# Performance work log

Hardware: AMD Instinct MI355X
Metric: run time of the kernel (lower is better)

## Reference

```python
import jax, jax.numpy as jnp
import numpy as np

N = 100000   # nodes
E = 1200000  # directed edges (avg degree 12)
D = 64       # in_feats
C = 40       # n_classes
K = 16       # propagation steps
ALPHA = 0.05


def setup_inputs() -> dict:
    key = jax.random.key(0)
    k1, k2, k3, k4 = jax.random.split(key, 4)
    feat = jax.random.normal(k1, (N, D), jnp.float32)
    # xavier_uniform for fc.weight [C, D]
    limit = np.sqrt(6.0 / (D + C)).astype(np.float32)
    W = jax.random.uniform(k2, (C, D), jnp.float32, -limit, limit)
    b = jnp.zeros((C,), jnp.float32)
    src = jax.random.randint(k3, (E,), 0, N, dtype=jnp.int32)
    dst = jax.random.randint(k4, (E,), 0, N, dtype=jnp.int32)
    return {"feat": feat, "W": W, "b": b, "src": src, "dst": dst}


def reference(feat, W, b, src, dst):
    # --- getNormAugAdj: A_hat = D^{-1/2} (A + I) D^{-1/2} ---
    loops = jnp.arange(N, dtype=src.dtype)
    row = jnp.concatenate([dst, loops])  # output node of each edge
    col = jnp.concatenate([src, loops])  # input  node of each edge
    ones = jnp.ones(row.shape, feat.dtype)
    deg = jax.ops.segment_sum(ones, row, num_segments=N)  # >= 1 (self-loops)
    dinv = jax.lax.rsqrt(deg)
    w = dinv[row] * dinv[col]  # per-edge normalized weight

    def spmm(x):  # x: [N, D] -> A_hat @ x
        return jax.ops.segment_sum(w[:, None] * x[col], row, num_segments=N)

    feat_ori = feat

    # SSGC loop (faithful to the original, including h /= K inside the loop)
    def step(carry, _):
        x, h = carry
        x = spmm(x)
        h = (h + (1.0 - ALPHA) * x + ALPHA * feat_ori) / K
        return (x, h), None

    (_, h), _ = jax.lax.scan(step, (feat, jnp.zeros_like(feat)), None, length=K)

    # fc(h)
    return h @ W.T + b
```

## Files before the change

### kernel.cpp

```cpp
#include <hip/hip_runtime.h>
#include <hip/hip_fp16.h>

#define NN 100000
#define EE 1200000
#define DD 64
#define CC 40
#define KK 16
#define BSZ 196
#define NBK 512
#define TCAP 3072
#define EPB 4096
#define ABLK ((EE + EPB - 1) / EPB)
#define PL1 (NN * 4)
#define GBLK ((NN + 11) / 12)

struct __align__(8) ERec { int c; float w; };

__global__ __launch_bounds__(512) void curinit_kernel(int* __restrict__ cursor) {
    int b = threadIdx.x;
    if (b < NBK) cursor[b] = b * TCAP;
}

__global__ __launch_bounds__(256) void sortA_kernel(const int* __restrict__ src,
                                                    const int* __restrict__ dst,
                                                    int* __restrict__ cursor,
                                                    int2* __restrict__ tmp) {
    __shared__ int2 stg[EPB];
    __shared__ int hist[NBK], loff[NBK], lcur[NBK], gbase[NBK];
    int t = threadIdx.x;
    long e0 = (long)blockIdx.x * EPB;
    int n = (int)((EE - e0 < EPB) ? (EE - e0) : EPB);
    for (int j = t; j < NBK; j += 256) hist[j] = 0;
    __syncthreads();
    int d[16], sx[16];
#pragma unroll
    for (int j = 0; j < 16; ++j) {
        int i = t + j * 256;
        if (i < n) {
            d[j] = dst[e0 + i];
            sx[j] = src[e0 + i];
            atomicAdd(&hist[d[j] / BSZ], 1);
        } else d[j] = -1;
    }
    __syncthreads();
    int c0 = hist[2 * t], c1 = hist[2 * t + 1];
    int s2 = c0 + c1;
    __syncthreads();
    loff[t] = s2;
    __syncthreads();
    for (int off = 1; off < 256; off <<= 1) {
        int u = (t >= off) ? loff[t - off] : 0;
        __syncthreads();
        loff[t] += u;
        __syncthreads();
    }
    int excl = loff[t] - s2;
    __syncthreads();
    loff[2 * t] = excl;          loff[2 * t + 1] = excl + c0;
    lcur[2 * t] = excl;          lcur[2 * t + 1] = excl + c0;
    gbase[2 * t]     = atomicAdd(&cursor[2 * t], c0);
    gbase[2 * t + 1] = atomicAdd(&cursor[2 * t + 1], c1);
    __syncthreads();
#pragma unroll
    for (int j = 0; j < 16; ++j) {
        if (d[j] >= 0) {
            int b = d[j] / BSZ;
            int p = atomicAdd(&lcur[b], 1);
            stg[p] = make_int2(d[j], sx[j]);
        }
    }
    __syncthreads();
    for (int i = t; i < n; i += 256) {
        int2 r = stg[i];
        int b = r.x / BSZ;
        int pos = gbase[b] + (i - loff[b]);
        if (pos < (b + 1) * TCAP) tmp[pos] = r;
    }
}

__global__ __launch_bounds__(512) void bscan_kernel(const int* __restrict__ cursor,
                                                    int* __restrict__ bbase,
                                                    int* __restrict__ row_ptr) {
    __shared__ int sm[512];
    int t = threadIdx.x;
    int v = (t < NBK) ? (cursor[t] - t * TCAP) : 0;
    sm[t] = v;
    __syncthreads();
    for (int off = 1; off < 512; off <<= 1) {
        int u = (t >= off) ? sm[t - off] : 0;
        __syncthreads();
        sm[t] += u;
        __syncthreads();
    }
    if (t < NBK) bbase[t] = sm[t] - v;
    if (t == 511) row_ptr[NN] = sm[511];
}

__global__ __launch_bounds__(256) void sortB_kernel(const int2* __restrict__ tmp,
                                                    const int* __restrict__ cursor,
                                                    const int* __restrict__ bbase,
                                                    float* __restrict__ dinv,
                                                    int* __restrict__ row_ptr,
                                                    int2* __restrict__ er2) {
    __shared__ int2 se[TCAP];
    __shared__ int2 so[TCAP];
    __shared__ int hist[256], lcur[256];
    int b = blockIdx.x;
    int n0 = b * BSZ;
    if (n0 >= NN) return;
    int n1 = n0 + BSZ; if (n1 > NN) n1 = NN;
    int nb = n1 - n0;
    int t = threadIdx.x;
    int cnt = cursor[b] - b * TCAP;
    int base = bbase[b];
    hist[t] = 0;
    __syncthreads();
    for (int i = t; i < cnt; i += 256) {
        int2 r = tmp[b * TCAP + i];
        se[i] = r;
        atomicAdd(&hist[r.x - n0], 1);
    }
    __syncthreads();
    if (t < nb) dinv[n0 + t] = rsqrtf((float)(hist[t] + 1));
    int v = hist[t];
    lcur[t] = v;
    __syncthreads();
    for (int off = 1; off < 256; off <<= 1) {
        int u = (t >= off) ? lcur[t - off] : 0;
        __syncthreads();
        lcur[t] += u;
        __syncthreads();
    }
    int excl = lcur[t] - v;
    __syncthreads();
    lcur[t] = excl;
    if (t < nb) row_ptr[n0 + t] = base + excl;
    __syncthreads();
    for (int i = t; i < cnt; i += 256) {
        int2 r = se[i];
        int ln = r.x - n0;
        int pos = atomicAdd(&lcur[ln], 1);
        so[pos] = make_int2(r.y, r.x);
    }
    __syncthreads();
    for (int i = t; i < cnt; i += 256) er2[base + i] = so[i];
}

__global__ __launch_bounds__(256) void wfill_kernel(const int2* __restrict__ er2,
                                                    const float* __restrict__ dinv,
                                                    int2* __restrict__ er) {
    int i = blockIdx.x * 256 + threadIdx.x;
    if (i >= EE) return;
    int2 r = er2[i];
    float w = dinv[r.y] * dinv[r.x];
    er[i] = make_int2(r.x, __float_as_int(w));
}

__global__ __launch_bounds__(256) void proj_kernel(const float4* __restrict__ feat4,
                                                   const float* __restrict__ W,
                                                   float4* __restrict__ y0) {
    __shared__ float smW[CC * 68];
    __shared__ float smF[64 * 68];
    __shared__ float smO[64 * 42];
    int t = threadIdx.x;
    for (int j = t; j < CC * 16; j += 256) {
        int c = j >> 4, q = j & 15;
        *(float4*)(smW + c * 68 + q * 4) = ((const float4*)W)[j];
    }
    int n0 = blockIdx.x * 64;
    for (int j = t; j < 64 * 16; j += 256) {
        int r = j >> 4, q = j & 15;
        if (n0 + r < NN)
            *(float4*)(smF + r * 68 + q * 4) = feat4[(size_t)(n0 + r) * 16 + q];
    }
    __syncthreads();
    int ln = t >> 2, c0 = (t & 3) * 10;
    int node = n0 + ln;
    float acc[10];
#pragma unroll
    for (int c = 0; c < 10; ++c) acc[c] = 0.f;
    if (node < NN) {
#pragma unroll
        for (int db = 0; db < 16; ++db) {
            float4 fv = *(const float4*)(smF + ln * 68 + db * 4);
#pragma unroll
            for (int c = 0; c < 10; ++c) {
                float4 wv = *(const float4*)(smW + (c0 + c) * 68 + db * 4);
                acc[c] = fmaf(fv.x, wv.x, acc[c]);
                acc[c] = fmaf(fv.y, wv.y, acc[c]);
                acc[c] = fmaf(fv.z, wv.z, acc[c]);
                acc[c] = fmaf(fv.w, wv.w, acc[c]);
            }
        }
    }
#pragma unroll
    for (int c = 0; c < 10; ++c) smO[ln * 42 + c0 + c] = acc[c];
    __syncthreads();
    for (int j = t; j < 64 * 5; j += 256) {
        int r = j / 5, q = j - r * 5;
        if (n0 + r < NN) {
            const float* s = smO + r * 42 + q * 8;
            float4 ov;
            __half2* op = (__half2*)&ov;
            op[0] = __floats2half2_rn(s[0], s[1]);
            op[1] = __floats2half2_rn(s[2], s[3]);
            op[2] = __floats2half2_rn(s[4], s[5]);
            op[3] = __floats2half2_rn(s[6], s[7]);
            y0[(q < 4) ? ((size_t)(n0 + r) * 4 + q) : (size_t)(PL1 + n0 + r)] = ov;
        }
    }
}

#define DEC8(V, F0, F1, F2, F3)                                             \
    const __half2* hp_##F0 = (const __half2*)&(V);                          \
    float2 F0 = __half22float2(hp_##F0[0]), F1 = __half22float2(hp_##F0[1]);\
    float2 F2 = __half22float2(hp_##F0[2]), F3 = __half22float2(hp_##F0[3]);

#define ACC8(R, V)                                                          \
    {                                                                       \
        DEC8(V, f0, f1, f2, f3)                                             \
        a0 = fmaf((R).w, f0.x, a0); a1 = fmaf((R).w, f0.y, a1);             \
        a2 = fmaf((R).w, f1.x, a2); a3 = fmaf((R).w, f1.y, a3);             \
        a4 = fmaf((R).w, f2.x, a4); a5 = fmaf((R).w, f2.y, a5);             \
        a6 = fmaf((R).w, f3.x, a6); a7 = fmaf((R).w, f3.y, a7);             \
    }

#define EDGE_LOOP                                                           \
    int e = beg;                                                            \
    int e8 = beg + ((end - beg) & ~7);                                      \
    for (; e < e8; e += 8) {                                                \
        ERec r0 = er[e], r1 = er[e + 1], r2 = er[e + 2], r3 = er[e + 3];    \
        ERec r4 = er[e + 4], r5 = er[e + 5], r6 = er[e + 6], r7 = er[e + 7];\
        float4 v0 = x[r0.c * m + a];                                        \
        float4 v1 = x[r1.c * m + a];                                        \
        float4 v2 = x[r2.c * m + a];                                        \
        float4 v3 = x[r3.c * m + a];                                        \
        float4 v4 = x[r4.c * m + a];                                        \
        float4 v5 = x[r5.c * m + a];                                        \
        float4 v6 = x[r6.c * m + a];                                        \
        float4 v7 = x[r7.c * m + a];                                        \
        ACC8(r0, v0); ACC8(r1, v1); ACC8(r2, v2); ACC8(r3, v3);             \
        ACC8(r4, v4); ACC8(r5, v5); ACC8(r6, v6); ACC8(r7, v7);             \
    }                                                                       \
    int e4 = e + ((end - e) & ~3);                                          \
    for (; e < e4; e += 4) {                                                \
        ERec r0 = er[e], r1 = er[e + 1], r2 = er[e + 2], r3 = er[e + 3];    \
        float4 v0 = x[r0.c * m + a];                                        \
        float4 v1 = x[r1.c * m + a];                                        \
        float4 v2 = x[r2.c * m + a];                                        \
        float4 v3 = x[r3.c * m + a];                                        \
        ACC8(r0, v0); ACC8(r1, v1); ACC8(r2, v2); ACC8(r3, v3);             \
    }                                                                       \
    for (; e < end; ++e) {                                                  \
        ERec r = er[e];                                                     \
        float4 v = x[r.c * m + a];                                          \
        ACC8(r, v);                                                         \
    }

__global__ __launch_bounds__(64) void spmm_prop(
    const float4* __restrict__ x, float4* __restrict__ x_out,
    const int* __restrict__ row_ptr, const ERec* __restrict__ er,
    const float* __restrict__ dinv) {
    int lane = threadIdx.x;
    int nw = lane / 5;
    int li = lane - nw * 5;
    int g = blockIdx.x * 12 + nw;
    if (nw >= 12 || g >= NN) return;
    int beg = row_ptr[g], end = row_ptr[g + 1];
    float di = dinv[g];
    float w0 = di * di;
    int m = (li < 4) ? 4 : 1;
    int a = (li < 4) ? li : PL1;
    int base = g * m + a;
    float4 sv = x[base];
    float a0, a1, a2, a3, a4, a5, a6, a7;
    {
        DEC8(sv, f0, f1, f2, f3)
        a0 = w0 * f0.x; a1 = w0 * f0.y; a2 = w0 * f1.x; a3 = w0 * f1.y;
        a4 = w0 * f2.x; a5 = w0 * f2.y; a6 = w0 * f3.x; a7 = w0 * f3.y;
    }
    EDGE_LOOP
    float4 ov;
    __half2* op = (__half2*)&ov;
    op[0] = __floats2half2_rn(a0, a1);
    op[1] = __floats2half2_rn(a2, a3);
    op[2] = __floats2half2_rn(a4, a5);
    op[3] = __floats2half2_rn(a6, a7);
    x_out[base] = ov;
}

__global__ __launch_bounds__(64) void spmm_final(
    const float4* __restrict__ x,
    const float4* __restrict__ x13p,
    const float4* __restrict__ x14p,
    const float4* __restrict__ y0,
    const float* __restrict__ bias,
    const int* __restrict__ row_ptr, const ERec* __restrict__ er,
    const float* __restrict__ dinv, float* __restrict__ outp) {
    int lane = threadIdx.x;
    int nw = lane / 5;
    int li = lane - nw * 5;
    int g = blockIdx.x * 12 + nw;
    if (nw >= 12 || g >= NN) return;
    int beg = row_ptr[g], end = row_ptr[g + 1];
    float di = dinv[g];
    float w0 = di * di;
    int m = (li < 4) ? 4 : 1;
    int a = (li < 4) ? li : PL1;
    int base = g * m + a;
    float4 sv = x[base];
    float s0, s1, s2, s3, s4, s5, s6, s7;
    float a0, a1, a2, a3, a4, a5, a6, a7;
    {
        DEC8(sv, f0, f1, f2, f3)
        s0 = f0.x; s1 = f0.y; s2 = f1.x; s3 = f1.y;
        s4 = f2.x; s5 = f2.y; s6 = f3.x; s7 = f3.y;
        a0 = w0 * s0; a1 = w0 * s1; a2 = w0 * s2; a3 = w0 * s3;
        a4 = w0 * s4; a5 = w0 * s5; a6 = w0 * s6; a7 = w0 * s7;
    }
    EDGE_LOOP
    const float C16 = 0.95f / 16.0f;
    const float C15 = 0.95f / 256.0f;
    const float C14 = 0.95f / 4096.0f;
    const float C13 = 0.95f / 65536.0f;
    const float FC  = 0.05f / 15.0f;
    float o0 = C16 * a0 + C15 * s0, o1 = C16 * a1 + C15 * s1;
    float o2 = C16 * a2 + C15 * s2, o3 = C16 * a3 + C15 * s3;
    float o4 = C16 * a4 + C15 * s4, o5 = C16 * a5 + C15 * s5;
    float o6 = C16 * a6 + C15 * s6, o7 = C16 * a7 + C15 * s7;
#define ADD8(P, CF)                                                         \
    {                                                                       \
        float4 v = (P)[base];                                               \
        DEC8(v, f0, f1, f2, f3)                                             \
        o0 = fmaf((CF), f0.x, o0); o1 = fmaf((CF), f0.y, o1);               \
        o2 = fmaf((CF), f1.x, o2); o3 = fmaf((CF), f1.y, o3);               \
        o4 = fmaf((CF), f2.x, o4); o5 = fmaf((CF), f2.y, o5);               \
        o6 = fmaf((CF), f3.x, o6); o7 = fmaf((CF), f3.y, o7);               \
    }
    ADD8(x14p, C14)
    ADD8(x13p, C13)
    ADD8(y0, FC)
#undef ADD8
    const float4* b4 = (const float4*)(bias + li * 8);
    float4 bb0 = b4[0], bb1 = b4[1];
    float4 w0v = make_float4(o0 + bb0.x, o1 + bb0.y, o2 + bb0.z, o3 + bb0.w);
    float4 w1v = make_float4(o4 + bb1.x, o5 + bb1.y, o6 + bb1.z, o7 + bb1.w);
    float4* op = (float4*)(outp + (size_t)g * CC + li * 8);
    op[0] = w0v; op[1] = w1v;
}

extern "C" void kernel_launch(void* const* d_in, const int* in_sizes, int n_in,
                              void* d_out, int out_size, void* d_ws, size_t ws_size,
                              hipStream_t stream) {
    const float* feat = (const float*)d_in[0];
    const float* W    = (const float*)d_in[1];
    const float* b    = (const float*)d_in[2];
    const int*   src  = (const int*)d_in[3];
    const int*   dst  = (const int*)d_in[4];
    float* out = (float*)d_out;

    char* p = (char*)d_ws;
    auto alloc = [&](size_t bytes) {
        char* r = p;
        p += (bytes + 255) & ~(size_t)255;
        return r;
    };
    float*   dinv    = (float*)alloc((size_t)NN * sizeof(float));
    int*     row_ptr = (int*)alloc((size_t)(NN + 1) * sizeof(int));
    int*     cursor  = (int*)alloc((size_t)NBK * sizeof(int));
    int*     bbase   = (int*)alloc((size_t)NBK * sizeof(int));
    int2*    tmp     = (int2*)alloc((size_t)NBK * TCAP * sizeof(int2));
    int2*    er2     = (int2*)alloc((size_t)EE * sizeof(int2));
    int2*    er      = (int2*)alloc((size_t)EE * sizeof(int2));
    float4*  y0      = (float4*)alloc((size_t)NN * 5 * sizeof(float4));
    float4*  xa      = (float4*)alloc((size_t)NN * 5 * sizeof(float4));
    float4*  xb      = (float4*)alloc((size_t)NN * 5 * sizeof(float4));
    float4*  x13b    = (float4*)alloc((size_t)NN * 5 * sizeof(float4));
    float4*  x14b    = (float4*)alloc((size_t)NN * 5 * sizeof(float4));
    float4*  x15b    = (float4*)alloc((size_t)NN * 5 * sizeof(float4));

    curinit_kernel<<<1, 512, 0, stream>>>(cursor);
    sortA_kernel<<<ABLK, 256, 0, stream>>>(src, dst, cursor, tmp);
    bscan_kernel<<<1, 512, 0, stream>>>(cursor, bbase, row_ptr);
    sortB_kernel<<<NBK, 256, 0, stream>>>(tmp, cursor, bbase, dinv, row_ptr, er2);
    wfill_kernel<<<(EE + 255) / 256, 256, 0, stream>>>(er2, dinv, er);
    proj_kernel<<<(NN + 63) / 64, 256, 0, stream>>>((const float4*)feat, W, y0);

    const float4* xs = y0;
    for (int j = 0; j < 12; ++j) {
        float4* xd = (j & 1) ? xb : xa;
        spmm_prop<<<GBLK, 64, 0, stream>>>(xs, xd, row_ptr, (const ERec*)er, dinv);
        xs = xd;
    }
    spmm_prop<<<GBLK, 64, 0, stream>>>(xs, x13b, row_ptr, (const ERec*)er, dinv);
    spmm_prop<<<GBLK, 64, 0, stream>>>(x13b, x14b, row_ptr, (const ERec*)er, dinv);
    spmm_prop<<<GBLK, 64, 0, stream>>>(x14b, x15b, row_ptr, (const ERec*)er, dinv);
    spmm_final<<<GBLK, 64, 0, stream>>>(x15b, x13b, x14b, y0, b, row_ptr,
                                        (const ERec*)er, dinv, out);
}
```

Measured before the change: 583.4 us.

## Split projected features into five column-plane arrays and remap SpMM blocks per plane

Stores the 40-wide half-precision projected features as five separate planes of 16-byte chunks, one per group of 8 classes, instead of four interleaved chunks plus a fifth plane. SpMM blocks now handle a plane pair (32 nodes × 2 chunks) or the last plane alone (64 nodes), instead of packing 12 nodes × 5 lanes into a 64-wide wave that left 4 lanes idle. The aim is full wave utilization and a smaller gather footprint per plane, which should help cache locality. The cost is that each edge's index and weight records are read separately per plane, so edge-list traffic goes up and rows of very different degree can share a wave.

```diff
diff --git a/kernel.cpp b/kernel.cpp
--- a/kernel.cpp
+++ b/kernel.cpp
@@ -11,8 +11,10 @@
 #define TCAP 3072
 #define EPB 4096
 #define ABLK ((EE + EPB - 1) / EPB)
-#define PL1 (NN * 4)
-#define GBLK ((NN + 11) / 12)
+
+#define NB2 3125
+#define NB1 1563
+#define GBLK2 (2 * NB2 + NB1)
 
 struct __align__(8) ERec { int c; float w; };
 
@@ -197,7 +199,7 @@
     for (int c = 0; c < 10; ++c) smO[ln * 42 + c0 + c] = acc[c];
     __syncthreads();
     for (int j = t; j < 64 * 5; j += 256) {
-        int r = j / 5, q = j - r * 5;
+        int r = j & 63, q = j >> 6;
         if (n0 + r < NN) {
             const float* s = smO + r * 42 + q * 8;
             float4 ov;
@@ -206,7 +208,7 @@
             op[1] = __floats2half2_rn(s[2], s[3]);
             op[2] = __floats2half2_rn(s[4], s[5]);
             op[3] = __floats2half2_rn(s[6], s[7]);
-            y0[(q < 4) ? ((size_t)(n0 + r) * 4 + q) : (size_t)(PL1 + n0 + r)] = ov;
+            y0[(size_t)q * NN + (n0 + r)] = ov;
         }
     }
 }
@@ -225,68 +227,75 @@
         a6 = fmaf((R).w, f3.x, a6); a7 = fmaf((R).w, f3.y, a7);             \
     }
 
-#define EDGE_LOOP                                                           \
+#define EDGE_LOOP(XP)                                                       \
     int e = beg;                                                            \
     int e8 = beg + ((end - beg) & ~7);                                      \
     for (; e < e8; e += 8) {                                                \
         ERec r0 = er[e], r1 = er[e + 1], r2 = er[e + 2], r3 = er[e + 3];    \
         ERec r4 = er[e + 4], r5 = er[e + 5], r6 = er[e + 6], r7 = er[e + 7];\
-        float4 v0 = x[r0.c * m + a];                                        \
-        float4 v1 = x[r1.c * m + a];                                        \
-        float4 v2 = x[r2.c * m + a];                                        \
-        float4 v3 = x[r3.c * m + a];                                        \
-        float4 v4 = x[r4.c * m + a];                                        \
-        float4 v5 = x[r5.c * m + a];                                        \
-        float4 v6 = x[r6.c * m + a];                                        \
-        float4 v7 = x[r7.c * m + a];                                        \
+        float4 v0 = (XP)[r0.c];                                             \
+        float4 v1 = (XP)[r1.c];                                             \
+        float4 v2 = (XP)[r2.c];                                             \
+        float4 v3 = (XP)[r3.c];                                             \
+        float4 v4 = (XP)[r4.c];                                             \
+        float4 v5 = (XP)[r5.c];                                             \
+        float4 v6 = (XP)[r6.c];                                             \
+        float4 v7 = (XP)[r7.c];                                             \
         ACC8(r0, v0); ACC8(r1, v1); ACC8(r2, v2); ACC8(r3, v3);             \
         ACC8(r4, v4); ACC8(r5, v5); ACC8(r6, v6); ACC8(r7, v7);             \
     }                                                                       \
     int e4 = e + ((end - e) & ~3);                                          \
     for (; e < e4; e += 4) {                                                \
         ERec r0 = er[e], r1 = er[e + 1], r2 = er[e + 2], r3 = er[e + 3];    \
-        float4 v0 = x[r0.c * m + a];                                        \
-        float4 v1 = x[r1.c * m + a];                                        \
-        float4 v2 = x[r2.c * m + a];                                        \
-        float4 v3 = x[r3.c * m + a];                                        \
+        float4 v0 = (XP)[r0.c];                                             \
+        float4 v1 = (XP)[r1.c];                                             \
+        float4 v2 = (XP)[r2.c];                                             \
+        float4 v3 = (XP)[r3.c];                                             \
         ACC8(r0, v0); ACC8(r1, v1); ACC8(r2, v2); ACC8(r3, v3);             \
     }                                                                       \
     for (; e < end; ++e) {                                                  \
         ERec r = er[e];                                                     \
-        float4 v = x[r.c * m + a];                                          \
+        float4 v = (XP)[r.c];                                               \
         ACC8(r, v);                                                         \
     }
+
+__device__ __forceinline__ bool bmap(int b, int lane, int& g, int& q) {
+    if (b < 2 * NB2) {
+        int pb = (b >= NB2) ? 1 : 0;
+        g = (b - pb * NB2) * 32 + (lane >> 1);
+        q = pb * 2 + (lane & 1);
+        return true;
+    }
+    g = (b - 2 * NB2) * 64 + lane;
+    q = 4;
+    return g < NN;
+}
 
 __global__ __launch_bounds__(64) void spmm_prop(
     const float4* __restrict__ x, float4* __restrict__ x_out,
     const int* __restrict__ row_ptr, const ERec* __restrict__ er,
     const float* __restrict__ dinv) {
-    int lane = threadIdx.x;
-    int nw = lane / 5;
-    int li = lane - nw * 5;
-    int g = blockIdx.x * 12 + nw;
-    if (nw >= 12 || g >= NN) return;
+    int g, q;
+    if (!bmap(blockIdx.x, threadIdx.x, g, q)) return;
+    const float4* xp = x + (size_t)q * NN;
     int beg = row_ptr[g], end = row_ptr[g + 1];
     float di = dinv[g];
     float w0 = di * di;
-    int m = (li < 4) ? 4 : 1;
-    int a = (li < 4) ? li : PL1;
-    int base = g * m + a;
-    float4 sv = x[base];
+    float4 sv = xp[g];
     float a0, a1, a2, a3, a4, a5, a6, a7;
     {
         DEC8(sv, f0, f1, f2, f3)
         a0 = w0 * f0.x; a1 = w0 * f0.y; a2 = w0 * f1.x; a3 = w0 * f1.y;
         a4 = w0 * f2.x; a5 = w0 * f2.y; a6 = w0 * f3.x; a7 = w0 * f3.y;
     }
-    EDGE_LOOP
+    EDGE_LOOP(xp)
     float4 ov;
     __half2* op = (__half2*)&ov;
     op[0] = __floats2half2_rn(a0, a1);
     op[1] = __floats2half2_rn(a2, a3);
     op[2] = __floats2half2_rn(a4, a5);
     op[3] = __floats2half2_rn(a6, a7);
-    x_out[base] = ov;
+    x_out[(size_t)q * NN + g] = ov;
 }
 
 __global__ __launch_bounds__(64) void spmm_final(
@@ -297,18 +306,14 @@
     const float* __restrict__ bias,
     const int* __restrict__ row_ptr, const ERec* __restrict__ er,
     const float* __restrict__ dinv, float* __restrict__ outp) {
-    int lane = threadIdx.x;
-    int nw = lane / 5;
-    int li = lane - nw * 5;
-    int g = blockIdx.x * 12 + nw;
-    if (nw >= 12 || g >= NN) return;
+    int g, q;
+    if (!bmap(blockIdx.x, threadIdx.x, g, q)) return;
+    const float4* xp = x + (size_t)q * NN;
+    size_t idx = (size_t)q * NN + g;
     int beg = row_ptr[g], end = row_ptr[g + 1];
     float di = dinv[g];
     float w0 = di * di;
-    int m = (li < 4) ? 4 : 1;
-    int a = (li < 4) ? li : PL1;
-    int base = g * m + a;
-    float4 sv = x[base];
+    float4 sv = xp[g];
     float s0, s1, s2, s3, s4, s5, s6, s7;
     float a0, a1, a2, a3, a4, a5, a6, a7;
     {
@@ -318,7 +323,7 @@
         a0 = w0 * s0; a1 = w0 * s1; a2 = w0 * s2; a3 = w0 * s3;
         a4 = w0 * s4; a5 = w0 * s5; a6 = w0 * s6; a7 = w0 * s7;
     }
-    EDGE_LOOP
+    EDGE_LOOP(xp)
     const float C16 = 0.95f / 16.0f;
     const float C15 = 0.95f / 256.0f;
     const float C14 = 0.95f / 4096.0f;
@@ -330,7 +335,7 @@
     float o6 = C16 * a6 + C15 * s6, o7 = C16 * a7 + C15 * s7;
 #define ADD8(P, CF)                                                         \
     {                                                                       \
-        float4 v = (P)[base];                                               \
+        float4 v = (P)[idx];                                                \
         DEC8(v, f0, f1, f2, f3)                                             \
         o0 = fmaf((CF), f0.x, o0); o1 = fmaf((CF), f0.y, o1);               \
         o2 = fmaf((CF), f1.x, o2); o3 = fmaf((CF), f1.y, o3);               \
@@ -341,11 +346,11 @@
     ADD8(x13p, C13)
     ADD8(y0, FC)
 #undef ADD8
-    const float4* b4 = (const float4*)(bias + li * 8);
+    const float4* b4 = (const float4*)(bias + q * 8);
     float4 bb0 = b4[0], bb1 = b4[1];
     float4 w0v = make_float4(o0 + bb0.x, o1 + bb0.y, o2 + bb0.z, o3 + bb0.w);
     float4 w1v = make_float4(o4 + bb1.x, o5 + bb1.y, o6 + bb1.z, o7 + bb1.w);
-    float4* op = (float4*)(outp + (size_t)g * CC + li * 8);
+    float4* op = (float4*)(outp + (size_t)g * CC + q * 8);
     op[0] = w0v; op[1] = w1v;
 }
 
@@ -389,12 +394,12 @@
     const float4* xs = y0;
     for (int j = 0; j < 12; ++j) {
         float4* xd = (j & 1) ? xb : xa;
-        spmm_prop<<<GBLK, 64, 0, stream>>>(xs, xd, row_ptr, (const ERec*)er, dinv);
+        spmm_prop<<<GBLK2, 64, 0, stream>>>(xs, xd, row_ptr, (const ERec*)er, dinv);
         xs = xd;
     }
-    spmm_prop<<<GBLK, 64, 0, stream>>>(xs, x13b, row_ptr, (const ERec*)er, dinv);
-    spmm_prop<<<GBLK, 64, 0, stream>>>(x13b, x14b, row_ptr, (const ERec*)er, dinv);
-    spmm_prop<<<GBLK, 64, 0, stream>>>(x14b, x15b, row_ptr, (const ERec*)er, dinv);
-    spmm_final<<<GBLK, 64, 0, stream>>>(x15b, x13b, x14b, y0, b, row_ptr,
-                                        (const ERec*)er, dinv, out);
-}
+    spmm_prop<<<GBLK2, 64, 0, stream>>>(xs, x13b, row_ptr, (const ERec*)er, dinv);
+    spmm_prop<<<GBLK2, 64, 0, stream>>>(x13b, x14b, row_ptr, (const ERec*)er, dinv);
+    spmm_prop<<<GBLK2, 64, 0, stream>>>(x14b, x15b, row_ptr, (const ERec*)er, dinv);
+    spmm_final<<<GBLK2, 64, 0, stream>>>(x15b, x13b, x14b, y0, b, row_ptr,
+                                         (const ERec*)er, dinv, out);
+}
```

After: 872.0 us. 1.49x slower.

## Propagate pre-scaled features with unweighted edges and XCD-aware plane partitioning

Applied to the files above, without the earlier changes.

Rescales the propagated state by D^{-1/2}, so each SpMM step is an unweighted neighbor sum followed by one per-node scale. Edges then store only the source index, which halves edge-list traffic and removes the weight-fill kernel. The feature layout is split into plane groups, and blocks are mapped by blockIdx mod 8 so each XCD handles one plane group and node range, aiming for better L2 locality of gathers. The final kernel undoes the scaling with sqrt(deg) and 1/sqrt(deg); fp16 storage of the scaled values may shift the rounding behaviour.

```diff
diff --git a/kernel.cpp b/kernel.cpp
--- a/kernel.cpp
+++ b/kernel.cpp
@@ -11,10 +11,10 @@
 #define TCAP 3072
 #define EPB 4096
 #define ABLK ((EE + EPB - 1) / EPB)
-#define PL1 (NN * 4)
-#define GBLK ((NN + 11) / 12)
-
-struct __align__(8) ERec { int c; float w; };
+
+#define NPX 1042
+#define NP4 782
+#define GRID8 (8 * NPX)
 
 __global__ __launch_bounds__(512) void curinit_kernel(int* __restrict__ cursor) {
     int b = threadIdx.x;
@@ -100,10 +100,11 @@
                                                     const int* __restrict__ cursor,
                                                     const int* __restrict__ bbase,
                                                     float* __restrict__ dinv,
+                                                    float* __restrict__ sqd,
                                                     int* __restrict__ row_ptr,
-                                                    int2* __restrict__ er2) {
+                                                    int* __restrict__ er_src) {
     __shared__ int2 se[TCAP];
-    __shared__ int2 so[TCAP];
+    __shared__ int so[TCAP];
     __shared__ int hist[256], lcur[256];
     int b = blockIdx.x;
     int n0 = b * BSZ;
@@ -121,7 +122,11 @@
         atomicAdd(&hist[r.x - n0], 1);
     }
     __syncthreads();
-    if (t < nb) dinv[n0 + t] = rsqrtf((float)(hist[t] + 1));
+    if (t < nb) {
+        float dg = (float)(hist[t] + 1);
+        dinv[n0 + t] = rsqrtf(dg);
+        sqd[n0 + t]  = sqrtf(dg);
+    }
     int v = hist[t];
     lcur[t] = v;
     __syncthreads();
@@ -140,25 +145,16 @@
         int2 r = se[i];
         int ln = r.x - n0;
         int pos = atomicAdd(&lcur[ln], 1);
-        so[pos] = make_int2(r.y, r.x);
-    }
-    __syncthreads();
-    for (int i = t; i < cnt; i += 256) er2[base + i] = so[i];
-}
-
-__global__ __launch_bounds__(256) void wfill_kernel(const int2* __restrict__ er2,
-                                                    const float* __restrict__ dinv,
-                                                    int2* __restrict__ er) {
-    int i = blockIdx.x * 256 + threadIdx.x;
-    if (i >= EE) return;
-    int2 r = er2[i];
-    float w = dinv[r.y] * dinv[r.x];
-    er[i] = make_int2(r.x, __float_as_int(w));
+        so[pos] = r.y;
+    }
+    __syncthreads();
+    for (int i = t; i < cnt; i += 256) er_src[base + i] = so[i];
 }
 
 __global__ __launch_bounds__(256) void proj_kernel(const float4* __restrict__ feat4,
                                                    const float* __restrict__ W,
-                                                   float4* __restrict__ y0) {
+                                                   const float* __restrict__ dinv,
+                                                   float4* __restrict__ z0) {
     __shared__ float smW[CC * 68];
     __shared__ float smF[64 * 68];
     __shared__ float smO[64 * 42];
@@ -197,16 +193,21 @@
     for (int c = 0; c < 10; ++c) smO[ln * 42 + c0 + c] = acc[c];
     __syncthreads();
     for (int j = t; j < 64 * 5; j += 256) {
-        int r = j / 5, q = j - r * 5;
-        if (n0 + r < NN) {
+        int r = j & 63, q = j >> 6;
+        int g = n0 + r;
+        if (g < NN) {
+            float dv = dinv[g];
             const float* s = smO + r * 42 + q * 8;
             float4 ov;
             __half2* op = (__half2*)&ov;
-            op[0] = __floats2half2_rn(s[0], s[1]);
-            op[1] = __floats2half2_rn(s[2], s[3]);
-            op[2] = __floats2half2_rn(s[4], s[5]);
-            op[3] = __floats2half2_rn(s[6], s[7]);
-            y0[(q < 4) ? ((size_t)(n0 + r) * 4 + q) : (size_t)(PL1 + n0 + r)] = ov;
+            op[0] = __floats2half2_rn(dv * s[0], dv * s[1]);
+            op[1] = __floats2half2_rn(dv * s[2], dv * s[3]);
+            op[2] = __floats2half2_rn(dv * s[4], dv * s[5]);
+            op[3] = __floats2half2_rn(dv * s[6], dv * s[7]);
+            size_t idx = (q < 2) ? ((size_t)g * 2 + q)
+                       : (q < 4) ? ((size_t)2 * NN + (size_t)g * 2 + (q - 2))
+                                 : ((size_t)4 * NN + g);
+            z0[idx] = ov;
         }
     }
 }
@@ -216,137 +217,183 @@
     float2 F0 = __half22float2(hp_##F0[0]), F1 = __half22float2(hp_##F0[1]);\
     float2 F2 = __half22float2(hp_##F0[2]), F3 = __half22float2(hp_##F0[3]);
 
-#define ACC8(R, V)                                                          \
+#define ACC8U(V)                                                            \
     {                                                                       \
         DEC8(V, f0, f1, f2, f3)                                             \
-        a0 = fmaf((R).w, f0.x, a0); a1 = fmaf((R).w, f0.y, a1);             \
-        a2 = fmaf((R).w, f1.x, a2); a3 = fmaf((R).w, f1.y, a3);             \
-        a4 = fmaf((R).w, f2.x, a4); a5 = fmaf((R).w, f2.y, a5);             \
-        a6 = fmaf((R).w, f3.x, a6); a7 = fmaf((R).w, f3.y, a7);             \
-    }
-
-#define EDGE_LOOP                                                           \
+        a0 += f0.x; a1 += f0.y; a2 += f1.x; a3 += f1.y;                     \
+        a4 += f2.x; a5 += f2.y; a6 += f3.x; a7 += f3.y;                     \
+    }
+
+#define GLOOP(XP, STR, PL)                                                  \
     int e = beg;                                                            \
     int e8 = beg + ((end - beg) & ~7);                                      \
     for (; e < e8; e += 8) {                                                \
-        ERec r0 = er[e], r1 = er[e + 1], r2 = er[e + 2], r3 = er[e + 3];    \
-        ERec r4 = er[e + 4], r5 = er[e + 5], r6 = er[e + 6], r7 = er[e + 7];\
-        float4 v0 = x[r0.c * m + a];                                        \
-        float4 v1 = x[r1.c * m + a];                                        \
-        float4 v2 = x[r2.c * m + a];                                        \
-        float4 v3 = x[r3.c * m + a];                                        \
-        float4 v4 = x[r4.c * m + a];                                        \
-        float4 v5 = x[r5.c * m + a];                                        \
-        float4 v6 = x[r6.c * m + a];                                        \
-        float4 v7 = x[r7.c * m + a];                                        \
-        ACC8(r0, v0); ACC8(r1, v1); ACC8(r2, v2); ACC8(r3, v3);             \
-        ACC8(r4, v4); ACC8(r5, v5); ACC8(r6, v6); ACC8(r7, v7);             \
+        int s0 = es[e], s1 = es[e + 1], s2 = es[e + 2], s3 = es[e + 3];     \
+        int s4 = es[e + 4], s5 = es[e + 5], s6 = es[e + 6], s7 = es[e + 7]; \
+        float4 v0 = (XP)[s0 * (STR) + (PL)];                                \
+        float4 v1 = (XP)[s1 * (STR) + (PL)];                                \
+        float4 v2 = (XP)[s2 * (STR) + (PL)];                                \
+        float4 v3 = (XP)[s3 * (STR) + (PL)];                                \
+        float4 v4 = (XP)[s4 * (STR) + (PL)];                                \
+        float4 v5 = (XP)[s5 * (STR) + (PL)];                                \
+        float4 v6 = (XP)[s6 * (STR) + (PL)];                                \
+        float4 v7 = (XP)[s7 * (STR) + (PL)];                                \
+        ACC8U(v0); ACC8U(v1); ACC8U(v2); ACC8U(v3);                         \
+        ACC8U(v4); ACC8U(v5); ACC8U(v6); ACC8U(v7);                         \
     }                                                                       \
     int e4 = e + ((end - e) & ~3);                                          \
     for (; e < e4; e += 4) {                                                \
-        ERec r0 = er[e], r1 = er[e + 1], r2 = er[e + 2], r3 = er[e + 3];    \
-        float4 v0 = x[r0.c * m + a];                                        \
-        float4 v1 = x[r1.c * m + a];                                        \
-        float4 v2 = x[r2.c * m + a];                                        \
-        float4 v3 = x[r3.c * m + a];                                        \
-        ACC8(r0, v0); ACC8(r1, v1); ACC8(r2, v2); ACC8(r3, v3);             \
+        int s0 = es[e], s1 = es[e + 1], s2 = es[e + 2], s3 = es[e + 3];     \
+        float4 v0 = (XP)[s0 * (STR) + (PL)];                                \
+        float4 v1 = (XP)[s1 * (STR) + (PL)];                                \
+        float4 v2 = (XP)[s2 * (STR) + (PL)];                                \
+        float4 v3 = (XP)[s3 * (STR) + (PL)];                                \
+        ACC8U(v0); ACC8U(v1); ACC8U(v2); ACC8U(v3);                         \
     }                                                                       \
     for (; e < end; ++e) {                                                  \
-        ERec r = er[e];                                                     \
-        float4 v = x[r.c * m + a];                                          \
-        ACC8(r, v);                                                         \
-    }
-
-__global__ __launch_bounds__(64) void spmm_prop(
+        int s = es[e];                                                      \
+        float4 v = (XP)[s * (STR) + (PL)];                                  \
+        ACC8U(v);                                                           \
+    }
+
+template <int STR>
+__device__ __forceinline__ void prop_body(
+    int g, int pl, size_t off,
     const float4* __restrict__ x, float4* __restrict__ x_out,
-    const int* __restrict__ row_ptr, const ERec* __restrict__ er,
+    const int* __restrict__ row_ptr, const int* __restrict__ es,
     const float* __restrict__ dinv) {
-    int lane = threadIdx.x;
-    int nw = lane / 5;
-    int li = lane - nw * 5;
-    int g = blockIdx.x * 12 + nw;
-    if (nw >= 12 || g >= NN) return;
+    const float4* xp = x + off;
     int beg = row_ptr[g], end = row_ptr[g + 1];
     float di = dinv[g];
-    float w0 = di * di;
-    int m = (li < 4) ? 4 : 1;
-    int a = (li < 4) ? li : PL1;
-    int base = g * m + a;
-    float4 sv = x[base];
+    float w2 = di * di;
+    int sb = g * STR + pl;
+    float4 sv = xp[sb];
     float a0, a1, a2, a3, a4, a5, a6, a7;
     {
         DEC8(sv, f0, f1, f2, f3)
-        a0 = w0 * f0.x; a1 = w0 * f0.y; a2 = w0 * f1.x; a3 = w0 * f1.y;
-        a4 = w0 * f2.x; a5 = w0 * f2.y; a6 = w0 * f3.x; a7 = w0 * f3.y;
-    }
-    EDGE_LOOP
+        a0 = f0.x; a1 = f0.y; a2 = f1.x; a3 = f1.y;
+        a4 = f2.x; a5 = f2.y; a6 = f3.x; a7 = f3.y;
+    }
+    GLOOP(xp, STR, pl)
     float4 ov;
     __half2* op = (__half2*)&ov;
-    op[0] = __floats2half2_rn(a0, a1);
-    op[1] = __floats2half2_rn(a2, a3);
-    op[2] = __floats2half2_rn(a4, a5);
-    op[3] = __floats2half2_rn(a6, a7);
-    x_out[base] = ov;
-}
-
-__global__ __launch_bounds__(64) void spmm_final(
-    const float4* __restrict__ x,
-    const float4* __restrict__ x13p,
-    const float4* __restrict__ x14p,
-    const float4* __restrict__ y0,
+    op[0] = __floats2half2_rn(w2 * a0, w2 * a1);
+    op[1] = __floats2half2_rn(w2 * a2, w2 * a3);
+    op[2] = __floats2half2_rn(w2 * a4, w2 * a5);
+    op[3] = __floats2half2_rn(w2 * a6, w2 * a7);
+    x_out[off + sb] = ov;
+}
+
+__global__ __launch_bounds__(64) void spmm_prop(
+    const float4* __restrict__ x, float4* __restrict__ x_out,
+    const int* __restrict__ row_ptr, const int* __restrict__ es,
+    const float* __restrict__ dinv) {
+    int xcd = blockIdx.x & 7;
+    int slot = blockIdx.x >> 3;
+    int lane = threadIdx.x;
+    if (xcd < 6) {
+        int part = (xcd < 3) ? xcd : xcd - 3;
+        int grp  = (xcd < 3) ? 0 : 1;
+        int b0 = (part == 0) ? 0 : ((part == 1) ? 33334 : 66667);
+        int b1 = (part == 0) ? 33334 : ((part == 1) ? 66667 : 100000);
+        int g = b0 + slot * 32 + (lane >> 1);
+        if (g >= b1) return;
+        prop_body<2>(g, lane & 1, (size_t)grp * 2 * NN, x, x_out, row_ptr, es, dinv);
+    } else {
+        if (slot >= NP4) return;
+        int b0 = (xcd - 6) * 50000;
+        int g = b0 + slot * 64 + lane;
+        if (g >= b0 + 50000) return;
+        prop_body<1>(g, 0, (size_t)4 * NN, x, x_out, row_ptr, es, dinv);
+    }
+}
+
+template <int STR>
+__device__ __forceinline__ void final_body(
+    int g, int pl, int p, size_t off,
+    const float4* __restrict__ x15, const float4* __restrict__ x13p,
+    const float4* __restrict__ x14p, const float4* __restrict__ z0p,
     const float* __restrict__ bias,
-    const int* __restrict__ row_ptr, const ERec* __restrict__ er,
-    const float* __restrict__ dinv, float* __restrict__ outp) {
-    int lane = threadIdx.x;
-    int nw = lane / 5;
-    int li = lane - nw * 5;
-    int g = blockIdx.x * 12 + nw;
-    if (nw >= 12 || g >= NN) return;
+    const int* __restrict__ row_ptr, const int* __restrict__ es,
+    const float* __restrict__ dinv, const float* __restrict__ sqd,
+    float* __restrict__ outp) {
+    const float4* xp = x15 + off;
     int beg = row_ptr[g], end = row_ptr[g + 1];
     float di = dinv[g];
-    float w0 = di * di;
-    int m = (li < 4) ? 4 : 1;
-    int a = (li < 4) ? li : PL1;
-    int base = g * m + a;
-    float4 sv = x[base];
+    float sq = sqd[g];
+    int sb = g * STR + pl;
+    size_t gi = off + sb;
+    float4 sv = xp[sb];
     float s0, s1, s2, s3, s4, s5, s6, s7;
     float a0, a1, a2, a3, a4, a5, a6, a7;
     {
         DEC8(sv, f0, f1, f2, f3)
         s0 = f0.x; s1 = f0.y; s2 = f1.x; s3 = f1.y;
         s4 = f2.x; s5 = f2.y; s6 = f3.x; s7 = f3.y;
-        a0 = w0 * s0; a1 = w0 * s1; a2 = w0 * s2; a3 = w0 * s3;
-        a4 = w0 * s4; a5 = w0 * s5; a6 = w0 * s6; a7 = w0 * s7;
-    }
-    EDGE_LOOP
+        a0 = s0; a1 = s1; a2 = s2; a3 = s3;
+        a4 = s4; a5 = s5; a6 = s6; a7 = s7;
+    }
+    GLOOP(xp, STR, pl)
     const float C16 = 0.95f / 16.0f;
     const float C15 = 0.95f / 256.0f;
     const float C14 = 0.95f / 4096.0f;
     const float C13 = 0.95f / 65536.0f;
     const float FC  = 0.05f / 15.0f;
-    float o0 = C16 * a0 + C15 * s0, o1 = C16 * a1 + C15 * s1;
-    float o2 = C16 * a2 + C15 * s2, o3 = C16 * a3 + C15 * s3;
-    float o4 = C16 * a4 + C15 * s4, o5 = C16 * a5 + C15 * s5;
-    float o6 = C16 * a6 + C15 * s6, o7 = C16 * a7 + C15 * s7;
-#define ADD8(P, CF)                                                         \
+    float t0 = C15 * s0, t1 = C15 * s1, t2 = C15 * s2, t3 = C15 * s3;
+    float t4 = C15 * s4, t5 = C15 * s5, t6 = C15 * s6, t7 = C15 * s7;
+#define ADD8T(P, CF)                                                        \
     {                                                                       \
-        float4 v = (P)[base];                                               \
+        float4 v = (P)[gi];                                                 \
         DEC8(v, f0, f1, f2, f3)                                             \
-        o0 = fmaf((CF), f0.x, o0); o1 = fmaf((CF), f0.y, o1);               \
-        o2 = fmaf((CF), f1.x, o2); o3 = fmaf((CF), f1.y, o3);               \
-        o4 = fmaf((CF), f2.x, o4); o5 = fmaf((CF), f2.y, o5);               \
-        o6 = fmaf((CF), f3.x, o6); o7 = fmaf((CF), f3.y, o7);               \
-    }
-    ADD8(x14p, C14)
-    ADD8(x13p, C13)
-    ADD8(y0, FC)
-#undef ADD8
-    const float4* b4 = (const float4*)(bias + li * 8);
+        t0 = fmaf((CF), f0.x, t0); t1 = fmaf((CF), f0.y, t1);               \
+        t2 = fmaf((CF), f1.x, t2); t3 = fmaf((CF), f1.y, t3);               \
+        t4 = fmaf((CF), f2.x, t4); t5 = fmaf((CF), f2.y, t5);               \
+        t6 = fmaf((CF), f3.x, t6); t7 = fmaf((CF), f3.y, t7);               \
+    }
+    ADD8T(x14p, C14)
+    ADD8T(x13p, C13)
+    ADD8T(z0p, FC)
+#undef ADD8T
+    float cd = C16 * di;
+    float o0 = fmaf(sq, t0, cd * a0), o1 = fmaf(sq, t1, cd * a1);
+    float o2 = fmaf(sq, t2, cd * a2), o3 = fmaf(sq, t3, cd * a3);
+    float o4 = fmaf(sq, t4, cd * a4), o5 = fmaf(sq, t5, cd * a5);
+    float o6 = fmaf(sq, t6, cd * a6), o7 = fmaf(sq, t7, cd * a7);
+    const float4* b4 = (const float4*)(bias + p * 8);
     float4 bb0 = b4[0], bb1 = b4[1];
-    float4 w0v = make_float4(o0 + bb0.x, o1 + bb0.y, o2 + bb0.z, o3 + bb0.w);
-    float4 w1v = make_float4(o4 + bb1.x, o5 + bb1.y, o6 + bb1.z, o7 + bb1.w);
-    float4* op = (float4*)(outp + (size_t)g * CC + li * 8);
-    op[0] = w0v; op[1] = w1v;
+    float4* op = (float4*)(outp + (size_t)g * CC + p * 8);
+    op[0] = make_float4(o0 + bb0.x, o1 + bb0.y, o2 + bb0.z, o3 + bb0.w);
+    op[1] = make_float4(o4 + bb1.x, o5 + bb1.y, o6 + bb1.z, o7 + bb1.w);
+}
+
+__global__ __launch_bounds__(64) void spmm_final(
+    const float4* __restrict__ x15, const float4* __restrict__ x13p,
+    const float4* __restrict__ x14p, const float4* __restrict__ z0p,
+    const float* __restrict__ bias,
+    const int* __restrict__ row_ptr, const int* __restrict__ es,
+    const float* __restrict__ dinv, const float* __restrict__ sqd,
+    float* __restrict__ outp) {
+    int xcd = blockIdx.x & 7;
+    int slot = blockIdx.x >> 3;
+    int lane = threadIdx.x;
+    if (xcd < 6) {
+        int part = (xcd < 3) ? xcd : xcd - 3;
+        int grp  = (xcd < 3) ? 0 : 1;
+        int b0 = (part == 0) ? 0 : ((part == 1) ? 33334 : 66667);
+        int b1 = (part == 0) ? 33334 : ((part == 1) ? 66667 : 100000);
+        int g = b0 + slot * 32 + (lane >> 1);
+        if (g >= b1) return;
+        int pl = lane & 1;
+        final_body<2>(g, pl, grp * 2 + pl, (size_t)grp * 2 * NN,
+                      x15, x13p, x14p, z0p, bias, row_ptr, es, dinv, sqd, outp);
+    } else {
+        if (slot >= NP4) return;
+        int b0 = (xcd - 6) * 50000;
+        int g = b0 + slot * 64 + lane;
+        if (g >= b0 + 50000) return;
+        final_body<1>(g, 0, 4, (size_t)4 * NN,
+                      x15, x13p, x14p, z0p, bias, row_ptr, es, dinv, sqd, outp);
+    }
 }
 
 extern "C" void kernel_launch(void* const* d_in, const int* in_sizes, int n_in,
@@ -366,35 +413,34 @@
         return r;
     };
     float*   dinv    = (float*)alloc((size_t)NN * sizeof(float));
+    float*   sqd     = (float*)alloc((size_t)NN * sizeof(float));
     int*     row_ptr = (int*)alloc((size_t)(NN + 1) * sizeof(int));
     int*     cursor  = (int*)alloc((size_t)NBK * sizeof(int));
     int*     bbase   = (int*)alloc((size_t)NBK * sizeof(int));
     int2*    tmp     = (int2*)alloc((size_t)NBK * TCAP * sizeof(int2));
-    int2*    er2     = (int2*)alloc((size_t)EE * sizeof(int2));
-    int2*    er      = (int2*)alloc((size_t)EE * sizeof(int2));
-    float4*  y0      = (float4*)alloc((size_t)NN * 5 * sizeof(float4));
+    int*     er_src  = (int*)alloc((size_t)EE * sizeof(int));
+    float4*  z0      = (float4*)alloc((size_t)NN * 5 * sizeof(float4));
     float4*  xa      = (float4*)alloc((size_t)NN * 5 * sizeof(float4));
     float4*  xb      = (float4*)alloc((size_t)NN * 5 * sizeof(float4));
-    float4*  x13b    = (float4*)alloc((size_t)NN * 5 * sizeof(float4));
-    float4*  x14b    = (float4*)alloc((size_t)NN * 5 * sizeof(float4));
-    float4*  x15b    = (float4*)alloc((size_t)NN * 5 * sizeof(float4));
+    float4*  z13     = (float4*)alloc((size_t)NN * 5 * sizeof(float4));
+    float4*  z14     = (float4*)alloc((size_t)NN * 5 * sizeof(float4));
+    float4*  z15     = (float4*)alloc((size_t)NN * 5 * sizeof(float4));
 
     curinit_kernel<<<1, 512, 0, stream>>>(cursor);
     sortA_kernel<<<ABLK, 256, 0, stream>>>(src, dst, cursor, tmp);
     bscan_kernel<<<1, 512, 0, stream>>>(cursor, bbase, row_ptr);
-    sortB_kernel<<<NBK, 256, 0, stream>>>(tmp, cursor, bbase, dinv, row_ptr, er2);
-    wfill_kernel<<<(EE + 255) / 256, 256, 0, stream>>>(er2, dinv, er);
-    proj_kernel<<<(NN + 63) / 64, 256, 0, stream>>>((const float4*)feat, W, y0);
-
-    const float4* xs = y0;
+    sortB_kernel<<<NBK, 256, 0, stream>>>(tmp, cursor, bbase, dinv, sqd, row_ptr, er_src);
+    proj_kernel<<<(NN + 63) / 64, 256, 0, stream>>>((const float4*)feat, W, dinv, z0);
+
+    const float4* xs = z0;
     for (int j = 0; j < 12; ++j) {
         float4* xd = (j & 1) ? xb : xa;
-        spmm_prop<<<GBLK, 64, 0, stream>>>(xs, xd, row_ptr, (const ERec*)er, dinv);
+        spmm_prop<<<GRID8, 64, 0, stream>>>(xs, xd, row_ptr, er_src, dinv);
         xs = xd;
     }
-    spmm_prop<<<GBLK, 64, 0, stream>>>(xs, x13b, row_ptr, (const ERec*)er, dinv);
-    spmm_prop<<<GBLK, 64, 0, stream>>>(x13b, x14b, row_ptr, (const ERec*)er, dinv);
-    spmm_prop<<<GBLK, 64, 0, stream>>>(x14b, x15b, row_ptr, (const ERec*)er, dinv);
-    spmm_final<<<GBLK, 64, 0, stream>>>(x15b, x13b, x14b, y0, b, row_ptr,
-                                        (const ERec*)er, dinv, out);
-}
+    spmm_prop<<<GRID8, 64, 0, stream>>>(xs, z13, row_ptr, er_src, dinv);
+    spmm_prop<<<GRID8, 64, 0, stream>>>(z13, z14, row_ptr, er_src, dinv);
+    spmm_prop<<<GRID8, 64, 0, stream>>>(z14, z15, row_ptr, er_src, dinv);
+    spmm_final<<<GRID8, 64, 0, stream>>>(z15, z13, z14, z0, b, row_ptr,
+                                         er_src, dinv, sqd, out);
+}
```

Measured after the change: 570.9 us. 2.1% less time.
